# Performance work log

Hardware: AMD Instinct MI355X
Metric: run time of the kernel (lower is better)

## Reference

```python
import jax, jax.numpy as jnp
import numpy as np

SEQ = 512; WIN = [4, 4, 4]; INNER = 5; DM = 256; H = 4; DK = 64; NEG = -1e9

def _all_sizes():
    s = [SEQ]
    for w in WIN:
        s.append(s[-1] // w)
    return s

def _build_mask():
    # Pyraformer get_mask: intra-scale band (inner_size) + inter-scale parent/child links.
    sizes = _all_sizes(); N = sum(sizes)
    starts = np.cumsum([0] + sizes)
    allow = np.zeros((N, N), bool)
    iw = INNER // 2
    for li, sz in enumerate(sizes):
        st = int(starts[li])
        for i in range(st, st + sz):
            allow[i, max(i - iw, st):min(i + iw + 1, st + sz)] = True
    for li in range(1, len(sizes)):
        st = int(starts[li])
        for i in range(st, st + sizes[li]):
            ls = int(starts[li - 1]) + (i - st) * WIN[li - 1]
            rs = st if i == st + sizes[li] - 1 else int(starts[li - 1]) + (i - st + 1) * WIN[li - 1]
            allow[i, ls:rs] = True
            allow[ls:rs, i] = True
    return jnp.asarray(~allow)  # True = blocked

def _build_indexes():
    # Pyraformer refer_points: for each base position, index of its node at every scale.
    sizes = _all_sizes(); starts = np.cumsum([0] + sizes)
    idx = np.zeros((SEQ, len(sizes)), np.int32)
    for i in range(SEQ):
        cur = i
        idx[i, 0] = cur
        for j in range(1, len(sizes)):
            inner = cur - int(starts[j - 1])
            cur = int(starts[j]) + min(inner // WIN[j - 1], sizes[j] - 1)
            idx[i, j] = cur
    return jnp.asarray(idx)

def _pos_enc(L, D):
    pos = np.arange(L)[:, None]
    div = np.exp(np.arange(0, D, 2) * (-np.log(10000.0) / D))
    pe = np.zeros((L, D), np.float32)
    pe[:, 0::2] = np.sin(pos * div)
    pe[:, 1::2] = np.cos(pos * div)
    return jnp.asarray(pe)

MASK = _build_mask()
INDEXES = _build_indexes()
PE = _pos_enc(SEQ, DM)
DN = ('NCH', 'OIH', 'NCH')

def _ln(x, g, b, eps=1e-5):
    m = x.mean(-1, keepdims=True)
    v = ((x - m) ** 2).mean(-1, keepdims=True)
    return (x - m) * jax.lax.rsqrt(v + eps) * g + b

def _forward(x_enc, x_mark, W_val, W_time, b_time, W_down, b_down, W_conv, b_conv, bn_g, bn_b, W_up, b_up, ln_c_g, ln_c_b, Wq, bq, Wk, bk, Wv, bv, Wo, bo, ln1_g, ln1_b, W1f, b1f, W2f, b2f, ln2_g, ln2_b, Wp, bp):
    B = x_enc.shape[0]
    # DataEmbedding: circular k=3 token conv + time-feature linear + fixed positional
    xt = jnp.pad(x_enc.transpose(0, 2, 1), ((0, 0), (0, 0), (1, 1)), mode='wrap')
    val = jax.lax.conv_general_dilated(xt, W_val, (1,), 'VALID', dimension_numbers=DN).transpose(0, 2, 1)
    emb = val + x_mark @ W_time + b_time + PE[None]  # [B, SEQ, DM]
    # CSCM Bottleneck_Construct: down-proj, strided conv pooling per scale, up-proj, concat, LN
    t = (emb @ W_down + b_down).transpose(0, 2, 1)  # [B, 64, SEQ]
    pooled = []
    for i in range(len(WIN)):
        t = jax.lax.conv_general_dilated(t, W_conv[i], (WIN[i],), 'VALID', dimension_numbers=DN) + b_conv[i][None, :, None]
        t = jax.nn.elu(t * bn_g[i][None, :, None] + bn_b[i][None, :, None])
        pooled.append(t)
    pooled = jnp.concatenate(pooled, axis=2).transpose(0, 2, 1) @ W_up + b_up  # [B, 168, DM]
    x = _ln(jnp.concatenate([emb, pooled], axis=1), ln_c_g, ln_c_b)  # [B, 680, DM]
    N = x.shape[1]
    scale = np.float32(1.0 / np.sqrt(DK))
    for l in range(Wq.shape[0]):
        q = (x @ Wq[l] + bq[l]).reshape(B, N, H, DK).transpose(0, 2, 1, 3)
        k = (x @ Wk[l] + bk[l]).reshape(B, N, H, DK).transpose(0, 2, 1, 3)
        v = (x @ Wv[l] + bv[l]).reshape(B, N, H, DK).transpose(0, 2, 1, 3)
        s = jnp.einsum('bhqd,bhkd->bhqk', q, k) * scale
        s = jnp.where(MASK[None, None], NEG, s)
        o = jnp.einsum('bhqk,bhkd->bhqd', jax.nn.softmax(s, axis=-1), v)
        o = o.transpose(0, 2, 1, 3).reshape(B, N, DM) @ Wo[l] + bo[l]
        x = _ln(x + o, ln1_g[l], ln1_b[l])  # post-norm (normalize_before=False)
        f = jax.nn.relu(x @ W1f[l] + b1f[l]) @ W2f[l] + b2f[l]
        x = _ln(x + f, ln2_g[l], ln2_b[l])
    # FC decoder path: gather each position's multi-scale nodes, concat features
    gathered = x[:, INDEXES.reshape(-1)].reshape(B, SEQ, -1)  # [B, SEQ, 4*DM]
    return gathered[:, -1] @ Wp + bp  # [B, 96]

def setup_inputs() -> dict:
    key = jax.random.key(0)
    ks = iter(jax.random.split(key, 64))
    def w(shape, s=0.05):
        return jax.random.normal(next(ks), shape, jnp.float32) * s
    d = {}
    d['x_enc'] = jax.random.normal(next(ks), (32, SEQ, 1), jnp.float32)
    d['x_mark'] = jax.random.normal(next(ks), (32, SEQ, 4), jnp.float32)
    d['W_val'] = w((DM, 1, 3))
    d['W_time'] = w((4, DM)); d['b_time'] = jnp.zeros((DM,), jnp.float32)
    d['W_down'] = w((DM, 64)); d['b_down'] = jnp.zeros((64,), jnp.float32)
    d['W_conv'] = w((3, 64, 64, 4)); d['b_conv'] = jnp.zeros((3, 64), jnp.float32)
    d['bn_g'] = jnp.ones((3, 64), jnp.float32); d['bn_b'] = jnp.zeros((3, 64), jnp.float32)
    d['W_up'] = w((64, DM)); d['b_up'] = jnp.zeros((DM,), jnp.float32)
    d['ln_c_g'] = jnp.ones((DM,), jnp.float32); d['ln_c_b'] = jnp.zeros((DM,), jnp.float32)
    d['Wq'] = w((2, DM, DM)); d['bq'] = jnp.zeros((2, DM), jnp.float32)
    d['Wk'] = w((2, DM, DM)); d['bk'] = jnp.zeros((2, DM), jnp.float32)
    d['Wv'] = w((2, DM, DM)); d['bv'] = jnp.zeros((2, DM), jnp.float32)
    d['Wo'] = w((2, DM, DM)); d['bo'] = jnp.zeros((2, DM), jnp.float32)
    d['ln1_g'] = jnp.ones((2, DM), jnp.float32); d['ln1_b'] = jnp.zeros((2, DM), jnp.float32)
    d['W1f'] = w((2, DM, 512)); d['b1f'] = jnp.zeros((2, 512), jnp.float32)
    d['W2f'] = w((2, 512, DM)); d['b2f'] = jnp.zeros((2, DM), jnp.float32)
    d['ln2_g'] = jnp.ones((2, DM), jnp.float32); d['ln2_b'] = jnp.zeros((2, DM), jnp.float32)
    d['Wp'] = w((4 * DM, 96)); d['bp'] = jnp.zeros((96,), jnp.float32)
    return d

def reference(x_enc, x_mark, W_val, W_time, b_time, W_down, b_down, W_conv, b_conv, bn_g, bn_b, W_up, b_up, ln_c_g, ln_c_b, Wq, bq, Wk, bk, Wv, bv, Wo, bo, ln1_g, ln1_b, W1f, b1f, W2f, b2f, ln2_g, ln2_b, Wp, bp):
    return _forward(x_enc, x_mark, W_val, W_time, b_time, W_down, b_down, W_conv, b_conv, bn_g, bn_b, W_up, b_up, ln_c_g, ln_c_b, Wq, bq, Wk, bk, Wv, bv, Wo, bo, ln1_g, ln1_b, W1f, b1f, W2f, b2f, ln2_g, ln2_b, Wp, bp)
```

## Files before the change

kernel.cpp:

```cpp
#include <hip/hip_runtime.h>
#include <hip/hip_bf16.h>
#include <math.h>

#define B 32
#define SEQ 512
#define NTOK 680
#define DM 256
#define FF 512
#define NROWS (B*NTOK)

using bf16x8 = __attribute__((ext_vector_type(8))) short;
using f32x4  = __attribute__((ext_vector_type(4))) float;
using u32x4  = __attribute__((ext_vector_type(4))) unsigned int;
typedef __hip_bfloat16 bf16;

__device__ __forceinline__ unsigned short f2bf(float f) {
    union { float f; unsigned u; } x; x.f = f;
    unsigned r = (x.u + 0x7fffu + ((x.u >> 16) & 1u)) >> 16;
    return (unsigned short)r;
}
__device__ __forceinline__ float bfu2f(unsigned short u) {
    union { unsigned u; float f; } x; x.u = ((unsigned)u) << 16;
    return x.f;
}
__device__ __forceinline__ void dotu(unsigned a, unsigned b, float& s) {
    union { unsigned u; float f; } al, ah, bl, bh;
    al.u = a << 16; ah.u = a & 0xffff0000u;
    bl.u = b << 16; bh.u = b & 0xffff0000u;
    s = fmaf(al.f, bl.f, s);
    s = fmaf(ah.f, bh.f, s);
}

__global__ __launch_bounds__(256) void emb_kernel(
    const float* __restrict__ x_enc, const float* __restrict__ x_mark,
    const float* __restrict__ W_val, const float* __restrict__ W_time,
    const float* __restrict__ b_time, float* __restrict__ X, bf16* __restrict__ Xe)
{
    int bs = blockIdx.x;
    int b = bs >> 9, s = bs & 511;
    int d = threadIdx.x;
    int sm1 = (s + 511) & 511, sp1 = (s + 1) & 511;
    float x0 = x_enc[b*512 + sm1];
    float x1 = x_enc[b*512 + s];
    float x2 = x_enc[b*512 + sp1];
    float val = x0 * W_val[d*3+0] + x1 * W_val[d*3+1] + x2 * W_val[d*3+2];
    const float* mk = &x_mark[(size_t)bs*4];
    float tm = mk[0]*W_time[d] + mk[1]*W_time[256+d] + mk[2]*W_time[512+d] + mk[3]*W_time[768+d];
    int i2 = d & ~1;
    float div = expf((float)i2 * (-9.210340371976184f / 256.0f));
    float ang = (float)s * div;
    float pe = (d & 1) ? cosf(ang) : sinf(ang);
    float out = val + tm + b_time[d] + pe;
    X[((size_t)(b*NTOK + s))*DM + d] = out;
    ((unsigned short*)Xe)[(size_t)bs*DM + d] = f2bf(out);
}

__global__ __launch_bounds__(64) void conv_kernel(
    const float* __restrict__ in, int inRPB, int inOff,
    float* __restrict__ Pool, int outOff, int Lout,
    const float* __restrict__ W_conv, const float* __restrict__ b_conv,
    const float* __restrict__ bn_g, const float* __restrict__ bn_b, int sc)
{
    __shared__ float lds[256];
    int blk = blockIdx.x;
    int b = blk / Lout, p = blk % Lout;
    int t = threadIdx.x;
    for (int u = t; u < 256; u += 64)
        lds[u] = in[((size_t)(b*inRPB + inOff + p*4 + (u >> 6)))*64 + (u & 63)];
    __syncthreads();
    float acc = b_conv[sc*64 + t];
    const float* w = &W_conv[(size_t)(sc*64 + t)*256];
    #pragma unroll 4
    for (int ci = 0; ci < 64; ++ci) {
        #pragma unroll
        for (int tap = 0; tap < 4; ++tap)
            acc = fmaf(lds[tap*64 + ci], w[ci*4 + tap], acc);
    }
    float v = acc * bn_g[sc*64 + t] + bn_b[sc*64 + t];
    v = v > 0.f ? v : expm1f(v);
    Pool[((size_t)(b*168 + outOff + p))*64 + t] = v;
}

__global__ __launch_bounds__(256) void up_kernel(
    const float* __restrict__ Pool, const float* __restrict__ W_up,
    const float* __restrict__ b_up, float* __restrict__ X)
{
    __shared__ float row[64];
    int blk = blockIdx.x;
    int b = blk / 168, p = blk % 168;
    int d = threadIdx.x;
    if (d < 64) row[d] = Pool[(size_t)blk*64 + d];
    __syncthreads();
    float acc = b_up[d];
    #pragma unroll 8
    for (int k = 0; k < 64; ++k) acc = fmaf(row[k], W_up[k*256 + d], acc);
    X[((size_t)(b*NTOK + 512 + p))*DM + d] = acc;
}

__global__ __launch_bounds__(256) void ln_kernel(
    const float* __restrict__ Xf, bf16* __restrict__ Xio,
    const float* __restrict__ g, const float* __restrict__ bta)
{
    int r = blockIdx.x*4 + (threadIdx.x >> 6);
    int lane = threadIdx.x & 63;
    float4 v = ((const float4*)(Xf + (size_t)r*DM))[lane];
    float s = v.x + v.y + v.z + v.w;
    #pragma unroll
    for (int o = 32; o; o >>= 1) s += __shfl_xor(s, o);
    float mean = s * (1.0f/256.0f);
    float dx = v.x-mean, dy = v.y-mean, dz = v.z-mean, dw = v.w-mean;
    float q = dx*dx + dy*dy + dz*dz + dw*dw;
    #pragma unroll
    for (int o = 32; o; o >>= 1) q += __shfl_xor(q, o);
    float inv = rsqrtf(q*(1.0f/256.0f) + 1e-5f);
    float4 gg = ((const float4*)g)[lane];
    float4 bb = ((const float4*)bta)[lane];
    float ox = dx*inv*gg.x + bb.x;
    float oy = dy*inv*gg.y + bb.y;
    float oz = dz*inv*gg.z + bb.z;
    float ow = dw*inv*gg.w + bb.w;
    unsigned u0 = (unsigned)f2bf(ox) | ((unsigned)f2bf(oy) << 16);
    unsigned u1 = (unsigned)f2bf(oz) | ((unsigned)f2bf(ow) << 16);
    ((uint2*)(Xio + (size_t)r*DM))[lane] = make_uint2(u0, u1);
}

__global__ void nbr_kernel(int* __restrict__ nbr, int* __restrict__ ncnt)
{
    int i = blockIdx.x * 64 + threadIdx.x;
    if (i >= NTOK) return;
    const int starts[5] = {0, 512, 640, 672, 680};
    int si = (i < 512) ? 0 : (i < 640) ? 1 : (i < 672) ? 2 : 3;
    int st = starts[si], en = starts[si+1];
    int idx = i - st;
    int cnt = 0;
    if (si >= 1) {
        int cs = starts[si-1] + idx*4;
        #pragma unroll
        for (int c = 0; c < 4; ++c) nbr[i*16 + cnt++] = cs + c;
    }
    int lo = (i-2 > st) ? i-2 : st;
    int hi = (i+2 < en-1) ? i+2 : en-1;
    for (int j = lo; j <= hi; ++j) nbr[i*16 + cnt++] = j;
    if (si <= 2) nbr[i*16 + cnt++] = starts[si+1] + (idx >> 2);
    ncnt[i] = cnt;
}

__global__ __launch_bounds__(256) void attn_kernel(
    const bf16* __restrict__ Q, const bf16* __restrict__ K,
    const bf16* __restrict__ V, bf16* __restrict__ O,
    const int* __restrict__ nbr, const int* __restrict__ ncnt)
{
    __shared__ float wsm[4][16];
    __shared__ int   jsm[4][16];
    int flat = blockIdx.x;
    int row = (flat & 7) * (NROWS/8) + (flat >> 3);
    int n = row % NTOK, b = row / NTOK;
    int h = threadIdx.x >> 6;
    int lane = threadIdx.x & 63;
    int j = lane >> 2, g = lane & 3;
    int cnt = ncnt[n];
    int nj = (j < cnt) ? nbr[n*16 + j] : n;
    int jr = b*NTOK + nj;

    const uint4* qp = (const uint4*)(Q + (size_t)row*DM + h*64 + g*16);
    const uint4* kp = (const uint4*)(K + (size_t)jr*DM + h*64 + g*16);
    uint4 qa = qp[0], qb = qp[1];
    uint4 ka = kp[0], kb = kp[1];
    float s = 0.f;
    dotu(qa.x, ka.x, s); dotu(qa.y, ka.y, s); dotu(qa.z, ka.z, s); dotu(qa.w, ka.w, s);
    dotu(qb.x, kb.x, s); dotu(qb.y, kb.y, s); dotu(qb.z, kb.z, s); dotu(qb.w, kb.w, s);
    s += __shfl_xor(s, 1);
    s += __shfl_xor(s, 2);
    s *= 0.125f;
    if (j >= cnt) s = -1e30f;
    float m = s;
    #pragma unroll
    for (int o = 4; o < 64; o <<= 1) m = fmaxf(m, __shfl_xor(m, o));
    float w = (j < cnt) ? expf(s - m) : 0.f;
    float den = w;
    #pragma unroll
    for (int o = 4; o < 64; o <<= 1) den += __shfl_xor(den, o);
    if (g == 0) { wsm[h][j] = w / den; jsm[h][j] = jr; }
    __syncthreads();

    float acc = 0.f;
    const unsigned short* Vu = (const unsigned short*)V;
    for (int jj = 0; jj < cnt; ++jj) {
        float wv = wsm[h][jj];
        int rr = jsm[h][jj];
        acc = fmaf(wv, bfu2f(Vu[(size_t)rr*DM + h*64 + lane]), acc);
    }
    ((unsigned short*)O)[(size_t)row*DM + h*64 + lane] = f2bf(acc);
}

struct WDesc { const float* src; bf16* dst; int K; int N; };
struct WTable { WDesc d[13]; };
__global__ __launch_bounds__(256) void wconv_kernel(WTable tbl)
{
    __shared__ float lds[32][33];
    WDesc ds = tbl.d[blockIdx.y];
    int ntn = ds.N >> 5;
    int ntiles = (ds.K >> 5) * ntn;
    int tile = blockIdx.x;
    if (tile >= ntiles) return;
    int k0 = (tile / ntn) * 32, n0 = (tile % ntn) * 32;
    int t = threadIdx.x;
    int r = t >> 3, c4 = (t & 7) * 4;
    float4 v = *(const float4*)(ds.src + (size_t)(k0 + r)*ds.N + n0 + c4);
    lds[r][c4+0] = v.x; lds[r][c4+1] = v.y; lds[r][c4+2] = v.z; lds[r][c4+3] = v.w;
    __syncthreads();
    unsigned u0 = (unsigned)f2bf(lds[c4+0][r]) | ((unsigned)f2bf(lds[c4+1][r]) << 16);
    unsigned u1 = (unsigned)f2bf(lds[c4+2][r]) | ((unsigned)f2bf(lds[c4+3][r]) << 16);
    *(uint2*)((unsigned short*)ds.dst + (size_t)(n0 + r)*ds.K + k0 + c4) = make_uint2(u0, u1);
}

#define CSTR 260
__global__ __launch_bounds__(256) void wo_ln_kernel(
    const bf16* __restrict__ Ob, bf16* __restrict__ Xh,
    const bf16* __restrict__ WoT, const float* __restrict__ bo,
    const float* __restrict__ g, const float* __restrict__ bta)
{
    __shared__ __align__(16) char smem[16384 + 33280];
    uint4* AsU = (uint4*)smem;
    const bf16x8* Asv = (const bf16x8*)smem;
    float* ctile = (float*)(smem + 16384);

    int t = threadIdx.x;
    int lane = t & 63, w = t >> 6;
    int nwg = gridDim.x;
    int wg = (blockIdx.x & 7) * (nwg >> 3) + (blockIdx.x >> 3);
    int row0 = wg * 32;
    const unsigned short* Obu = (const unsigned short*)Ob;
    const unsigned short* Xu  = (const unsigned short*)Xh;
    const unsigned short* Wu  = (const unsigned short*)WoT;

    #pragma unroll
    for (int i = 0; i < 4; ++i) {
        int gg = t + i*256, r = gg >> 5, c = gg & 31;
        AsU[r*32 + (c ^ (r & 7))] = *(const uint4*)(Obu + (size_t)(row0 + r)*DM + c*8);
    }

    f32x4 acc[2][4];
    #pragma unroll
    for (int m = 0; m < 2; ++m)
        #pragma unroll
        for (int nn = 0; nn < 4; ++nn)
            #pragma unroll
            for (int q = 0; q < 4; ++q) acc[m][nn][q] = 0.f;
    float bv[4];
    #pragma unroll
    for (int nn = 0; nn < 4; ++nn) bv[nn] = bo[w*64 + nn*16 + (lane & 15)];
    __syncthreads();

    #pragma unroll
    for (int kt = 0; kt < 256; kt += 32) {
        int cg = (kt >> 3) + (lane >> 4);
        bf16x8 af[2];
        #pragma unroll
        for (int m = 0; m < 2; ++m) {
            int ar = m*16 + (lane & 15);
            af[m] = Asv[ar*32 + (cg ^ (ar & 7))];
        }
        #pragma unroll
        for (int nn = 0; nn < 4; ++nn) {
            int nrow = w*64 + nn*16 + (lane & 15);
            bf16x8 bfr = *(const bf16x8*)(Wu + (size_t)nrow*256 + kt + (lane >> 4)*8);
            #pragma unroll
            for (int m = 0; m < 2; ++m)
                acc[m][nn] = __builtin_amdgcn_mfma_f32_16x16x32_bf16(af[m], bfr, acc[m][nn], 0, 0, 0);
        }
    }

    __syncthreads();
    #pragma unroll
    for (int m = 0; m < 2; ++m)
        #pragma unroll
        for (int nn = 0; nn < 4; ++nn) {
            int col = w*64 + nn*16 + (lane & 15);
            #pragma unroll
            for (int q = 0; q < 4; ++q) {
                int row = m*16 + (lane >> 4)*4 + q;
                ctile[row*CSTR + col] = acc[m][nn][q] + bv[nn];
            }
        }
    __syncthreads();
    #pragma unroll
    for (int rr = 0; rr < 8; ++rr) {
        int row = w*8 + rr;
        float4 v = *(const float4*)(ctile + row*CSTR + lane*4);
        uint2 xu = *(const uint2*)(Xu + (size_t)(row0 + row)*DM + lane*4);
        v.x += bfu2f((unsigned short)(xu.x & 0xffffu));
        v.y += bfu2f((unsigned short)(xu.x >> 16));
        v.z += bfu2f((unsigned short)(xu.y & 0xffffu));
        v.w += bfu2f((unsigned short)(xu.y >> 16));
        float s = v.x + v.y + v.z + v.w;
        #pragma unroll
        for (int o = 32; o; o >>= 1) s += __shfl_xor(s, o);
        float mean = s * (1.0f/256.0f);
        float dx = v.x-mean, dy = v.y-mean, dz = v.z-mean, dw = v.w-mean;
        float q2 = dx*dx + dy*dy + dz*dz + dw*dw;
        #pragma unroll
        for (int o = 32; o; o >>= 1) q2 += __shfl_xor(q2, o);
        float inv = rsqrtf(q2*(1.0f/256.0f) + 1e-5f);
        float4 gg = ((const float4*)g)[lane];
        float4 bb = ((const float4*)bta)[lane];
        float ox = dx*inv*gg.x + bb.x;
        float oy = dy*inv*gg.y + bb.y;
        float oz = dz*inv*gg.z + bb.z;
        float ow = dw*inv*gg.w + bb.w;
        unsigned u0 = (unsigned)f2bf(ox) | ((unsigned)f2bf(oy) << 16);
        unsigned u1 = (unsigned)f2bf(oz) | ((unsigned)f2bf(ow) << 16);
        *(uint2*)((unsigned short*)Xh + (size_t)(row0 + row)*DM + lane*4) = make_uint2(u0, u1);
    }
}

#define HSTR 280
__global__ __launch_bounds__(256) void ff_kernel(
    bf16* __restrict__ Xh,
    const bf16* __restrict__ W1t, const float* __restrict__ b1,
    const bf16* __restrict__ W2t, const float* __restrict__ b2,
    const float* __restrict__ g, const float* __restrict__ bta)
{
    __shared__ __align__(16) char smem[16384 + 33280];
    uint4* AsU = (uint4*)smem;
    const bf16x8* Asv = (const bf16x8*)smem;
    unsigned short* hT = (unsigned short*)(smem + 16384);
    float* ctile = (float*)(smem + 16384);

    int t = threadIdx.x;
    int lane = t & 63, w = t >> 6;
    int nwg = gridDim.x;
    int wg = (blockIdx.x & 7) * (nwg >> 3) + (blockIdx.x >> 3);
    int row0 = wg * 32;
    const unsigned short* Xu = (const unsigned short*)Xh;

    #pragma unroll
    for (int i = 0; i < 4; ++i) {
        int gg = t + i*256, r = gg >> 5, c = gg & 31;
        AsU[r*32 + (c ^ (r & 7))] = *(const uint4*)(Xu + (size_t)(row0 + r)*DM + c*8);
    }

    f32x4 acc2[2][4];
    #pragma unroll
    for (int m = 0; m < 2; ++m)
        #pragma unroll
        for (int nn = 0; nn < 4; ++nn)
            #pragma unroll
            for (int q = 0; q < 4; ++q) acc2[m][nn][q] = 0.f;
    float b2v[4];
    #pragma unroll
    for (int nn = 0; nn < 4; ++nn) b2v[nn] = b2[w*64 + nn*16 + (lane & 15)];
    __syncthreads();

    const unsigned short* W1u = (const unsigned short*)W1t;
    const unsigned short* W2u = (const unsigned short*)W2t;

    #pragma unroll
    for (int half = 0; half < 2; ++half) {
        f32x4 acc1[2][4];
        #pragma unroll
        for (int m = 0; m < 2; ++m)
            #pragma unroll
            for (int nn = 0; nn < 4; ++nn)
                #pragma unroll
                for (int q = 0; q < 4; ++q) acc1[m][nn][q] = 0.f;
        #pragma unroll
        for (int kt = 0; kt < 256; kt += 32) {
            int cg = (kt >> 3) + (lane >> 4);
            bf16x8 af[2];
            #pragma unroll
            for (int m = 0; m < 2; ++m) {
                int ar = m*16 + (lane & 15);
                af[m] = Asv[ar*32 + (cg ^ (ar & 7))];
            }
            #pragma unroll
            for (int nn = 0; nn < 4; ++nn) {
                int nrow = half*256 + w*64 + nn*16 + (lane & 15);
                bf16x8 bfr = *(const bf16x8*)(W1u + (size_t)nrow*256 + kt + (lane >> 4)*8);
                #pragma unroll
                for (int m = 0; m < 2; ++m)
                    acc1[m][nn] = __builtin_amdgcn_mfma_f32_16x16x32_bf16(af[m], bfr, acc1[m][nn], 0, 0, 0);
            }
        }
        float b1v[4];
        #pragma unroll
        for (int nn = 0; nn < 4; ++nn) b1v[nn] = b1[half*256 + w*64 + nn*16 + (lane & 15)];
        __syncthreads();
        #pragma unroll
        for (int m = 0; m < 2; ++m)
            #pragma unroll
            for (int nn = 0; nn < 4; ++nn) {
                int col = w*64 + nn*16 + (lane & 15);
                #pragma unroll
                for (int q = 0; q < 4; ++q) {
                    int row = m*16 + (lane >> 4)*4 + q;
                    hT[row*HSTR + col] = f2bf(fmaxf(acc1[m][nn][q] + b1v[nn], 0.f));
                }
            }
        __syncthreads();
        #pragma unroll
        for (int kt = 0; kt < 256; kt += 32) {
            bf16x8 af[2];
            #pragma unroll
            for (int m = 0; m < 2; ++m) {
                int ar = m*16 + (lane & 15);
                af[m] = *(const bf16x8*)(hT + ar*HSTR + kt + (lane >> 4)*8);
            }
            #pragma unroll
            for (int nn = 0; nn < 4; ++nn) {
                int nrow = w*64 + nn*16 + (lane & 15);
                bf16x8 bfr = *(const bf16x8*)(W2u + (size_t)nrow*512 + half*256 + kt + (lane >> 4)*8);
                #pragma unroll
                for (int m = 0; m < 2; ++m)
                    acc2[m][nn] = __builtin_amdgcn_mfma_f32_16x16x32_bf16(af[m], bfr, acc2[m][nn], 0, 0, 0);
            }
        }
    }
    __syncthreads();
    #pragma unroll
    for (int m = 0; m < 2; ++m)
        #pragma unroll
        for (int nn = 0; nn < 4; ++nn) {
            int col = w*64 + nn*16 + (lane & 15);
            #pragma unroll
            for (int q = 0; q < 4; ++q) {
                int row = m*16 + (lane >> 4)*4 + q;
                ctile[row*CSTR + col] = acc2[m][nn][q] + b2v[nn];
            }
        }
    __syncthreads();
    #pragma unroll
    for (int rr = 0; rr < 8; ++rr) {
        int row = w*8 + rr;
        float4 v = *(const float4*)(ctile + row*CSTR + lane*4);
        uint2 xu = *(const uint2*)(Xu + (size_t)(row0 + row)*DM + lane*4);
        v.x += bfu2f((unsigned short)(xu.x & 0xffffu));
        v.y += bfu2f((unsigned short)(xu.x >> 16));
        v.z += bfu2f((unsigned short)(xu.y & 0xffffu));
        v.w += bfu2f((unsigned short)(xu.y >> 16));
        float s = v.x + v.y + v.z + v.w;
        #pragma unroll
        for (int o = 32; o; o >>= 1) s += __shfl_xor(s, o);
        float mean = s * (1.0f/256.0f);
        float dx = v.x-mean, dy = v.y-mean, dz = v.z-mean, dw = v.w-mean;
        float q2 = dx*dx + dy*dy + dz*dz + dw*dw;
        #pragma unroll
        for (int o = 32; o; o >>= 1) q2 += __shfl_xor(q2, o);
        float inv = rsqrtf(q2*(1.0f/256.0f) + 1e-5f);
        float4 gg = ((const float4*)g)[lane];
        float4 bb = ((const float4*)bta)[lane];
        float ox = dx*inv*gg.x + bb.x;
        float oy = dy*inv*gg.y + bb.y;
        float oz = dz*inv*gg.z + bb.z;
        float ow = dw*inv*gg.w + bb.w;
        unsigned u0 = (unsigned)f2bf(ox) | ((unsigned)f2bf(oy) << 16);
        unsigned u1 = (unsigned)f2bf(oz) | ((unsigned)f2bf(ow) << 16);
        *(uint2*)((unsigned short*)Xh + (size_t)(row0 + row)*DM + lane*4) = make_uint2(u0, u1);
    }
}

template<int KD, int NY, int NZ, bool RELU>
__global__ __launch_bounds__(256) void mfma_gemm_fr(
    const bf16* __restrict__ A,
    const bf16* __restrict__ Wt0, const bf16* __restrict__ Wt1, const bf16* __restrict__ Wt2,
    const float* __restrict__ b0, const float* __restrict__ b1, const float* __restrict__ b2,
    bf16* __restrict__ O0, bf16* __restrict__ O1, bf16* __restrict__ O2,
    int Nc, int totalWg)
{
    __shared__ __align__(16) char smem[40960];
    uint4* AsU = (uint4*)smem;
    uint4* BsU = (uint4*)(smem + 8192);
    const bf16x8* Asv = (const bf16x8*)smem;
    const bf16x8* Bsv = (const bf16x8*)(smem + 8192);

    int t = threadIdx.x;
    int lane = t & 63, wid = t >> 6;
    int nwg = gridDim.x;
    int wg = (blockIdx.x & 7) * (nwg >> 3) + (blockIdx.x >> 3);
    if (wg >= totalWg) return;
    int xt = wg / (NY*NZ);
    int rem = wg % (NY*NZ);
    int z = rem / NY;
    int y = rem % NY;
    int row0 = xt * 64;
    int n0 = y * 256;
    const bf16* W = ((z == 0) ? Wt0 : (z == 1) ? Wt1 : Wt2) + (size_t)n0*KD;
    const float* bias = (z == 0) ? b0 : (z == 1) ? b1 : b2;
    bf16* Op = (z == 0) ? O0 : (z == 1) ? O1 : O2;

    f32x4 acc[4][4];
    #pragma unroll
    for (int i = 0; i < 4; ++i)
        #pragma unroll
        for (int jn = 0; jn < 4; ++jn)
            #pragma unroll
            for (int r = 0; r < 4; ++r) acc[i][jn][r] = 0.f;

    uint4 pa[2], pb[8];
    #pragma unroll
    for (int i = 0; i < 2; ++i) {
        int gg = t + i*256, r = gg >> 3, c = gg & 7;
        pa[i] = *reinterpret_cast<const uint4*>(A + (size_t)(row0 + r)*KD + c*8);
    }
    #pragma unroll
    for (int i = 0; i < 8; ++i) {
        int gg = t + i*256, r = gg >> 3, c = gg & 7;
        pb[i] = *reinterpret_cast<const uint4*>(W + (size_t)r*KD + c*8);
    }

    #pragma unroll
    for (int kt = 0; kt < KD; kt += 64) {
        __syncthreads();
        #pragma unroll
        for (int i = 0; i < 2; ++i) {
            int gg = t + i*256, r = gg >> 3, c = gg & 7;
            AsU[r*8 + (c ^ (r & 7))] = pa[i];
        }
        #pragma unroll
        for (int i = 0; i < 8; ++i) {
            int gg = t + i*256, r = gg >> 3, c = gg & 7;
            BsU[r*8 + (c ^ (r & 7))] = pb[i];
        }
        __syncthreads();
        if (kt + 64 < KD) {
            #pragma unroll
            for (int i = 0; i < 2; ++i) {
                int gg = t + i*256, r = gg >> 3, c = gg & 7;
                pa[i] = *reinterpret_cast<const uint4*>(A + (size_t)(row0 + r)*KD + (kt + 64) + c*8);
            }
            #pragma unroll
            for (int i = 0; i < 8; ++i) {
                int gg = t + i*256, r = gg >> 3, c = gg & 7;
                pb[i] = *reinterpret_cast<const uint4*>(W + (size_t)r*KD + (kt + 64) + c*8);
            }
        }
        #pragma unroll
        for (int ks = 0; ks < 2; ++ks) {
            int cg = ks*4 + (lane >> 4);
            bf16x8 af[4], bfr[4];
            #pragma unroll
            for (int m = 0; m < 4; ++m) {
                int ar = m*16 + (lane & 15);
                af[m] = Asv[ar*8 + (cg ^ (ar & 7))];
            }
            #pragma unroll
            for (int nn = 0; nn < 4; ++nn) {
                int br = wid*64 + nn*16 + (lane & 15);
                bfr[nn] = Bsv[br*8 + (cg ^ (br & 7))];
            }
            #pragma unroll
            for (int m = 0; m < 4; ++m)
                #pragma unroll
                for (int nn = 0; nn < 4; ++nn)
                    acc[m][nn] = __builtin_amdgcn_mfma_f32_16x16x32_bf16(af[m], bfr[nn], acc[m][nn], 0, 0, 0);
        }
    }

    __syncthreads();
    unsigned short* ctb = (unsigned short*)smem;
    #pragma unroll
    for (int m = 0; m < 4; ++m) {
        #pragma unroll
        for (int nn = 0; nn < 4; ++nn) {
            int cc = wid*64 + nn*16 + (lane & 15);
            float bcol = bias[n0 + cc];
            #pragma unroll
            for (int r = 0; r < 4; ++r) {
                int rr = m*16 + (lane >> 4)*4 + r;
                float v = acc[m][nn][r] + bcol;
                if (RELU) v = fmaxf(v, 0.f);
                ctb[rr*264 + cc] = f2bf(v);
            }
        }
    }
    __syncthreads();
    #pragma unroll
    for (int i = 0; i < 8; ++i) {
        int idx = t + i*256;
        int row = idx >> 5, c16 = idx & 31;
        u32x4 uv = *(const u32x4*)(ctb + row*264 + c16*8);
        *(u32x4*)((unsigned short*)Op + (size_t)(row0 + row)*Nc + n0 + c16*8) = uv;
    }
}

__global__ __launch_bounds__(256) void mfma_gemm_dn(
    const bf16* __restrict__ A, const bf16* __restrict__ Wt,
    const float* __restrict__ bias, float* __restrict__ Op)
{
    __shared__ __align__(16) char smem[34816];
    uint4* AsU = (uint4*)smem;
    uint4* BsU = (uint4*)(smem + 16384);
    const bf16x8* Asv = (const bf16x8*)smem;
    const bf16x8* Bsv = (const bf16x8*)(smem + 16384);
    const int KD = 256, Nc = 64;

    int t = threadIdx.x;
    int lane = t & 63, wid = t >> 6;
    int wm = wid >> 1, wn = wid & 1;
    int nwg = gridDim.x;
    int wg = (blockIdx.x & 7) * (nwg >> 3) + (blockIdx.x >> 3);
    int row0 = wg * 128;
    int n0 = 0;

    f32x4 acc[4][2];
    #pragma unroll
    for (int i = 0; i < 4; ++i)
        #pragma unroll
        for (int jn = 0; jn < 2; ++jn)
            #pragma unroll
            for (int r = 0; r < 4; ++r) acc[i][jn][r] = 0.f;

    uint4 pa[4], pb[2];
    #pragma unroll
    for (int i = 0; i < 4; ++i) {
        int gg = t + i*256, r = gg >> 3, c = gg & 7;
        pa[i] = *reinterpret_cast<const uint4*>(A + (size_t)(row0 + r)*KD + c*8);
    }
    #pragma unroll
    for (int i = 0; i < 2; ++i) {
        int gg = t + i*256, r = gg >> 3, c = gg & 7;
        pb[i] = *reinterpret_cast<const uint4*>(Wt + (size_t)(n0 + r)*KD + c*8);
    }

    #pragma unroll
    for (int kt = 0; kt < KD; kt += 64) {
        __syncthreads();
        #pragma unroll
        for (int i = 0; i < 4; ++i) {
            int gg = t + i*256, r = gg >> 3, c = gg & 7;
            AsU[r*8 + (c ^ (r & 7))] = pa[i];
        }
        #pragma unroll
        for (int i = 0; i < 2; ++i) {
            int gg = t + i*256, r = gg >> 3, c = gg & 7;
            BsU[r*8 + (c ^ (r & 7))] = pb[i];
        }
        __syncthreads();
        if (kt + 64 < KD) {
            #pragma unroll
            for (int i = 0; i < 4; ++i) {
                int gg = t + i*256, r = gg >> 3, c = gg & 7;
                pa[i] = *reinterpret_cast<const uint4*>(A + (size_t)(row0 + r)*KD + (kt + 64) + c*8);
            }
            #pragma unroll
            for (int i = 0; i < 2; ++i) {
                int gg = t + i*256, r = gg >> 3, c = gg & 7;
                pb[i] = *reinterpret_cast<const uint4*>(Wt + (size_t)(n0 + r)*KD + (kt + 64) + c*8);
            }
        }
        #pragma unroll
        for (int ks = 0; ks < 2; ++ks) {
            int cg = ks*4 + (lane >> 4);
            bf16x8 af[4], bfr[2];
            #pragma unroll
            for (int m = 0; m < 4; ++m) {
                int ar = wm*64 + m*16 + (lane & 15);
                af[m] = Asv[ar*8 + (cg ^ (ar & 7))];
            }
            #pragma unroll
            for (int nn = 0; nn < 2; ++nn) {
                int br = wn*32 + nn*16 + (lane & 15);
                bfr[nn] = Bsv[br*8 + (cg ^ (br & 7))];
            }
            #pragma unroll
            for (int m = 0; m < 4; ++m)
                #pragma unroll
                for (int nn = 0; nn < 2; ++nn)
                    acc[m][nn] = __builtin_amdgcn_mfma_f32_16x16x32_bf16(af[m], bfr[nn], acc[m][nn], 0, 0, 0);
        }
    }

    __syncthreads();
    float* ctile = (float*)smem;
    #pragma unroll
    for (int m = 0; m < 4; ++m) {
        #pragma unroll
        for (int nn = 0; nn < 2; ++nn) {
            int cc = wn*32 + nn*16 + (lane & 15);
            float bcol = bias[n0 + cc];
            #pragma unroll
            for (int r = 0; r < 4; ++r) {
                int rr = wm*64 + m*16 + (lane >> 4)*4 + r;
                ctile[rr*68 + cc] = acc[m][nn][r] + bcol;
            }
        }
    }
    __syncthreads();
    int c4 = (t & 15) * 4;
    #pragma unroll
    for (int rr = t >> 4; rr < 128; rr += 16) {
        float4 v = *reinterpret_cast<const float4*>(ctile + rr*68 + c4);
        *reinterpret_cast<float4*>(Op + (size_t)(row0 + rr)*Nc + n0 + c4) = v;
    }
}

__global__ __launch_bounds__(128) void final_kernel(
    const bf16* __restrict__ Xh, const float* __restrict__ Wp,
    const float* __restrict__ bp, float* __restrict__ out)
{
    __shared__ float rows[1024];
    int b = blockIdx.x, t = threadIdx.x;
    const unsigned short* Xu = (const unsigned short*)Xh;
    for (int u = t; u < 1024; u += 128) {
        int g = u >> 8;
        int id = (g == 0) ? 511 : (g == 1) ? 639 : (g == 2) ? 671 : 679;
        rows[u] = bfu2f(Xu[((size_t)(b*NTOK + id))*DM + (u & 255)]);
    }
    __syncthreads();
    if (t < 96) {
        float acc = bp[t];
        #pragma unroll 8
        for (int k = 0; k < 1024; ++k) acc = fmaf(rows[k], Wp[k*96 + t], acc);
        out[b*96 + t] = acc;
    }
}

extern "C" void kernel_launch(void* const* d_in, const int* in_sizes, int n_in,
                              void* d_out, int out_size, void* d_ws, size_t ws_size,
                              hipStream_t stream)
{
    const float* x_enc  = (const float*)d_in[0];
    const float* x_mark = (const float*)d_in[1];
    const float* W_val  = (const float*)d_in[2];
    const float* W_time = (const float*)d_in[3];
    const float* b_time = (const float*)d_in[4];
    const float* W_down = (const float*)d_in[5];
    const float* b_down = (const float*)d_in[6];
    const float* W_conv = (const float*)d_in[7];
    const float* b_conv = (const float*)d_in[8];
    const float* bn_g   = (const float*)d_in[9];
    const float* bn_b   = (const float*)d_in[10];
    const float* W_up   = (const float*)d_in[11];
    const float* b_up   = (const float*)d_in[12];
    const float* ln_c_g = (const float*)d_in[13];
    const float* ln_c_b = (const float*)d_in[14];
    const float* Wq     = (const float*)d_in[15];
    const float* bq     = (const float*)d_in[16];
    const float* Wk     = (const float*)d_in[17];
    const float* bk     = (const float*)d_in[18];
    const float* Wv     = (const float*)d_in[19];
    const float* bv     = (const float*)d_in[20];
    const float* Wo     = (const float*)d_in[21];
    const float* bo     = (const float*)d_in[22];
    const float* ln1_g  = (const float*)d_in[23];
    const float* ln1_b  = (const float*)d_in[24];
    const float* W1f    = (const float*)d_in[25];
    const float* b1f    = (const float*)d_in[26];
    const float* W2f    = (const float*)d_in[27];
    const float* b2f    = (const float*)d_in[28];
    const float* ln2_g  = (const float*)d_in[29];
    const float* ln2_b  = (const float*)d_in[30];
    const float* Wp     = (const float*)d_in[31];
    const float* bp     = (const float*)d_in[32];

    const size_t RB = (size_t)NROWS * DM;
    float* ws = (float*)d_ws;
    float* X    = ws;
    float* Td   = X + RB;
    float* Pool = Td + (size_t)B*SEQ*64;
    bf16* bws   = (bf16*)(Pool + (size_t)B*168*64);
    bf16* Xh   = bws;
    bf16* Qh   = Xh  + RB;
    bf16* Kh   = Qh  + RB;
    bf16* Vh   = Kh  + RB;
    bf16* Obh  = Vh  + RB;
    bf16* Xe   = Obh + RB;
    bf16* WqT  = Xe  + (size_t)B*SEQ*DM;
    bf16* WkT  = WqT + 2*65536;
    bf16* WvT  = WkT + 2*65536;
    bf16* WoT  = WvT + 2*65536;
    bf16* W1T  = WoT + 2*65536;
    bf16* W2T  = W1T + 2*131072;
    bf16* WdT  = W2T + 2*131072;
    int*  nbr  = (int*)(WdT + 64*256);
    int*  ncnt = nbr + NTOK*16;

    WTable tbl;
    for (int l = 0; l < 2; ++l) {
        tbl.d[l*6+0] = { Wq  + (size_t)l*65536,  WqT + (size_t)l*65536,  256, 256 };
        tbl.d[l*6+1] = { Wk  + (size_t)l*65536,  WkT + (size_t)l*65536,  256, 256 };
        tbl.d[l*6+2] = { Wv  + (size_t)l*65536,  WvT + (size_t)l*65536,  256, 256 };
        tbl.d[l*6+3] = { Wo  + (size_t)l*65536,  WoT + (size_t)l*65536,  256, 256 };
        tbl.d[l*6+4] = { W1f + (size_t)l*131072, W1T + (size_t)l*131072, 256, 512 };
        tbl.d[l*6+5] = { W2f + (size_t)l*131072, W2T + (size_t)l*131072, 512, 256 };
    }
    tbl.d[12] = { W_down, WdT, 256, 64 };
    wconv_kernel<<<dim3(128, 13), 256, 0, stream>>>(tbl);

    emb_kernel<<<B*SEQ, 256, 0, stream>>>(x_enc, x_mark, W_val, W_time, b_time, X, Xe);
    mfma_gemm_dn<<<128, 256, 0, stream>>>(Xe, WdT, b_down, Td);
    conv_kernel<<<B*128, 64, 0, stream>>>(Td, 512, 0,   Pool, 0,   128, W_conv, b_conv, bn_g, bn_b, 0);
    conv_kernel<<<B*32,  64, 0, stream>>>(Pool, 168, 0,  Pool, 128, 32,  W_conv, b_conv, bn_g, bn_b, 1);
    conv_kernel<<<B*8,   64, 0, stream>>>(Pool, 168, 128,Pool, 160, 8,   W_conv, b_conv, bn_g, bn_b, 2);
    up_kernel<<<B*168, 256, 0, stream>>>(Pool, W_up, b_up, X);
    ln_kernel<<<NROWS/4, 256, 0, stream>>>(X, Xh, ln_c_g, ln_c_b);
    nbr_kernel<<<11, 64, 0, stream>>>(nbr, ncnt);

    const int MT = NROWS/64;
    for (int l = 0; l < 2; ++l) {
        const bf16* wqt = WqT + (size_t)l*65536;
        const bf16* wkt = WkT + (size_t)l*65536;
        const bf16* wvt = WvT + (size_t)l*65536;
        const bf16* wot = WoT + (size_t)l*65536;
        const bf16* w1t = W1T + (size_t)l*131072;
        const bf16* w2t = W2T + (size_t)l*131072;
        const float* bq_ = bq + l*DM; const float* bk_ = bk + l*DM;
        const float* bv_ = bv + l*DM; const float* bo_ = bo + l*DM;
        const float* b1_ = b1f + l*FF; const float* b2_ = b2f + l*DM;

        mfma_gemm_fr<256,1,3,false><<<1024, 256, 0, stream>>>(
            Xh, wqt, wkt, wvt, bq_, bk_, bv_, Qh, Kh, Vh, 256, MT*3);
        attn_kernel<<<NROWS, 256, 0, stream>>>(Qh, Kh, Vh, Obh, nbr, ncnt);
        wo_ln_kernel<<<680, 256, 0, stream>>>(Obh, Xh, wot, bo_, ln1_g + l*DM, ln1_b + l*DM);
        ff_kernel<<<680, 256, 0, stream>>>(Xh, w1t, b1_, w2t, b2_, ln2_g + l*DM, ln2_b + l*DM);
    }

    final_kernel<<<B, 128, 0, stream>>>(Xh, Wp, bp, (float*)d_out);
}
```

Measured before the change: 471.0 us.

## Fold Wv·Wo per head and fuse attention with output projection and LN

```diff
diff --git a/kernel.cpp b/kernel.cpp
--- a/kernel.cpp
+++ b/kernel.cpp
@@ -145,56 +145,8 @@
     ncnt[i] = cnt;
 }
 
-__global__ __launch_bounds__(256) void attn_kernel(
-    const bf16* __restrict__ Q, const bf16* __restrict__ K,
-    const bf16* __restrict__ V, bf16* __restrict__ O,
-    const int* __restrict__ nbr, const int* __restrict__ ncnt)
-{
-    __shared__ float wsm[4][16];
-    __shared__ int   jsm[4][16];
-    int flat = blockIdx.x;
-    int row = (flat & 7) * (NROWS/8) + (flat >> 3);
-    int n = row % NTOK, b = row / NTOK;
-    int h = threadIdx.x >> 6;
-    int lane = threadIdx.x & 63;
-    int j = lane >> 2, g = lane & 3;
-    int cnt = ncnt[n];
-    int nj = (j < cnt) ? nbr[n*16 + j] : n;
-    int jr = b*NTOK + nj;
-
-    const uint4* qp = (const uint4*)(Q + (size_t)row*DM + h*64 + g*16);
-    const uint4* kp = (const uint4*)(K + (size_t)jr*DM + h*64 + g*16);
-    uint4 qa = qp[0], qb = qp[1];
-    uint4 ka = kp[0], kb = kp[1];
-    float s = 0.f;
-    dotu(qa.x, ka.x, s); dotu(qa.y, ka.y, s); dotu(qa.z, ka.z, s); dotu(qa.w, ka.w, s);
-    dotu(qb.x, kb.x, s); dotu(qb.y, kb.y, s); dotu(qb.z, kb.z, s); dotu(qb.w, kb.w, s);
-    s += __shfl_xor(s, 1);
-    s += __shfl_xor(s, 2);
-    s *= 0.125f;
-    if (j >= cnt) s = -1e30f;
-    float m = s;
-    #pragma unroll
-    for (int o = 4; o < 64; o <<= 1) m = fmaxf(m, __shfl_xor(m, o));
-    float w = (j < cnt) ? expf(s - m) : 0.f;
-    float den = w;
-    #pragma unroll
-    for (int o = 4; o < 64; o <<= 1) den += __shfl_xor(den, o);
-    if (g == 0) { wsm[h][j] = w / den; jsm[h][j] = jr; }
-    __syncthreads();
-
-    float acc = 0.f;
-    const unsigned short* Vu = (const unsigned short*)V;
-    for (int jj = 0; jj < cnt; ++jj) {
-        float wv = wsm[h][jj];
-        int rr = jsm[h][jj];
-        acc = fmaf(wv, bfu2f(Vu[(size_t)rr*DM + h*64 + lane]), acc);
-    }
-    ((unsigned short*)O)[(size_t)row*DM + h*64 + lane] = f2bf(acc);
-}
-
 struct WDesc { const float* src; bf16* dst; int K; int N; };
-struct WTable { WDesc d[13]; };
+struct WTable { WDesc d[9]; };
 __global__ __launch_bounds__(256) void wconv_kernel(WTable tbl)
 {
     __shared__ float lds[32][33];
@@ -214,31 +166,103 @@
     *(uint2*)((unsigned short*)ds.dst + (size_t)(n0 + r)*ds.K + k0 + c4) = make_uint2(u0, u1);
 }
 
+__global__ __launch_bounds__(256) void wvo_kernel(
+    const float* __restrict__ Wv, const float* __restrict__ Wo, bf16* __restrict__ WvoT)
+{
+    int lh = blockIdx.y; int l = lh >> 2, h = lh & 3;
+    int e = blockIdx.x*256 + threadIdx.x;
+    int n = e >> 8, k = e & 255;
+    const float* wv = Wv + (size_t)l*65536 + k*256 + h*64;
+    const float* wo = Wo + (size_t)l*65536 + (h*64)*256 + n;
+    float acc = 0.f;
+    #pragma unroll 8
+    for (int m = 0; m < 64; ++m) acc = fmaf(wv[m], wo[m*256], acc);
+    ((unsigned short*)WvoT)[(size_t)lh*65536 + n*256 + k] = f2bf(acc);
+}
+
+__global__ void fvec_kernel(const float* __restrict__ bv, const float* __restrict__ Wo,
+                            const float* __restrict__ bo, float* __restrict__ fvec)
+{
+    int l = blockIdx.x, n = threadIdx.x;
+    const float* bvl = bv + l*256;
+    const float* wol = Wo + (size_t)l*65536;
+    float acc = bo[l*256 + n];
+    for (int c = 0; c < 256; ++c) acc = fmaf(bvl[c], wol[c*256 + n], acc);
+    fvec[l*256 + n] = acc;
+}
+
+#define HSTR 280
 #define CSTR 260
-__global__ __launch_bounds__(256) void wo_ln_kernel(
-    const bf16* __restrict__ Ob, bf16* __restrict__ Xh,
-    const bf16* __restrict__ WoT, const float* __restrict__ bo,
-    const float* __restrict__ g, const float* __restrict__ bta)
-{
-    __shared__ __align__(16) char smem[16384 + 33280];
-    uint4* AsU = (uint4*)smem;
-    const bf16x8* Asv = (const bf16x8*)smem;
-    float* ctile = (float*)(smem + 16384);
+__global__ __launch_bounds__(256) void attn_full_kernel(
+    const bf16* __restrict__ Qh, const bf16* __restrict__ Kh,
+    const bf16* __restrict__ Xin, bf16* __restrict__ Xout,
+    const bf16* __restrict__ WvoT,
+    const float* __restrict__ fvec,
+    const float* __restrict__ g, const float* __restrict__ bta,
+    const int* __restrict__ nbr, const int* __restrict__ ncnt)
+{
+    __shared__ __align__(16) char smem[33280 + 8192 + 2048 + 128];
+    unsigned short* Ysm = (unsigned short*)smem;
+    float* ctile = (float*)smem;
+    float* Psm  = (float*)(smem + 33280);
+    int* jrowS  = (int*)(smem + 33280 + 8192);
+    int* cntS   = (int*)(smem + 33280 + 8192 + 2048);
 
     int t = threadIdx.x;
-    int lane = t & 63, w = t >> 6;
+    int w = t >> 6, lane = t & 63;
     int nwg = gridDim.x;
     int wg = (blockIdx.x & 7) * (nwg >> 3) + (blockIdx.x >> 3);
     int row0 = wg * 32;
-    const unsigned short* Obu = (const unsigned short*)Ob;
-    const unsigned short* Xu  = (const unsigned short*)Xh;
-    const unsigned short* Wu  = (const unsigned short*)WoT;
-
-    #pragma unroll
-    for (int i = 0; i < 4; ++i) {
-        int gg = t + i*256, r = gg >> 5, c = gg & 31;
-        AsU[r*32 + (c ^ (r & 7))] = *(const uint4*)(Obu + (size_t)(row0 + r)*DM + c*8);
-    }
+    const unsigned short* Qu = (const unsigned short*)Qh;
+    const unsigned short* Ku = (const unsigned short*)Kh;
+    const unsigned short* Xu = (const unsigned short*)Xin;
+    const unsigned short* Wu = (const unsigned short*)WvoT;
+
+    if (t < 32) cntS[t] = ncnt[(row0 + t) % NTOK];
+    #pragma unroll
+    for (int i = 0; i < 2; ++i) {
+        int idx = t + i*256, r = idx >> 4, s = idx & 15;
+        int grow = row0 + r;
+        int n = grow % NTOK, b = grow / NTOK;
+        int c = ncnt[n];
+        jrowS[r*16 + s] = (s < c) ? (b*NTOK + nbr[n*16 + s]) : grow;
+    }
+    __syncthreads();
+
+    {
+        int s = lane >> 2, gd = lane & 3;
+        for (int rr = 0; rr < 8; ++rr) {
+            int r = w*8 + rr, grow = row0 + r;
+            int cnt = cntS[r];
+            int jr = jrowS[r*16 + s];
+            bool valid = s < cnt;
+            #pragma unroll
+            for (int h = 0; h < 4; ++h) {
+                const uint4* qp = (const uint4*)(Qu + (size_t)grow*DM + h*64 + gd*16);
+                const uint4* kp = (const uint4*)(Ku + (size_t)jr*DM + h*64 + gd*16);
+                uint4 qa = qp[0], qb = qp[1];
+                uint4 ka = kp[0], kb = kp[1];
+                float sv = 0.f;
+                dotu(qa.x, ka.x, sv); dotu(qa.y, ka.y, sv);
+                dotu(qa.z, ka.z, sv); dotu(qa.w, ka.w, sv);
+                dotu(qb.x, kb.x, sv); dotu(qb.y, kb.y, sv);
+                dotu(qb.z, kb.z, sv); dotu(qb.w, kb.w, sv);
+                sv += __shfl_xor(sv, 1);
+                sv += __shfl_xor(sv, 2);
+                sv *= 0.125f;
+                if (!valid) sv = -1e30f;
+                float m = sv;
+                #pragma unroll
+                for (int o = 4; o < 64; o <<= 1) m = fmaxf(m, __shfl_xor(m, o));
+                float p = valid ? expf(sv - m) : 0.f;
+                float den = p;
+                #pragma unroll
+                for (int o = 4; o < 64; o <<= 1) den += __shfl_xor(den, o);
+                if (gd == 0) Psm[(r*4 + h)*16 + s] = p / den;
+            }
+        }
+    }
+    __syncthreads();
 
     f32x4 acc[2][4];
     #pragma unroll
@@ -247,31 +271,63 @@
         for (int nn = 0; nn < 4; ++nn)
             #pragma unroll
             for (int q = 0; q < 4; ++q) acc[m][nn][q] = 0.f;
-    float bv[4];
-    #pragma unroll
-    for (int nn = 0; nn < 4; ++nn) bv[nn] = bo[w*64 + nn*16 + (lane & 15)];
-    __syncthreads();
-
-    #pragma unroll
-    for (int kt = 0; kt < 256; kt += 32) {
-        int cg = (kt >> 3) + (lane >> 4);
-        bf16x8 af[2];
-        #pragma unroll
-        for (int m = 0; m < 2; ++m) {
-            int ar = m*16 + (lane & 15);
-            af[m] = Asv[ar*32 + (cg ^ (ar & 7))];
-        }
-        #pragma unroll
-        for (int nn = 0; nn < 4; ++nn) {
-            int nrow = w*64 + nn*16 + (lane & 15);
-            bf16x8 bfr = *(const bf16x8*)(Wu + (size_t)nrow*256 + kt + (lane >> 4)*8);
-            #pragma unroll
-            for (int m = 0; m < 2; ++m)
-                acc[m][nn] = __builtin_amdgcn_mfma_f32_16x16x32_bf16(af[m], bfr, acc[m][nn], 0, 0, 0);
-        }
-    }
-
-    __syncthreads();
+
+    int rY = t >> 3, dg = t & 7;
+    #pragma unroll
+    for (int h = 0; h < 4; ++h) {
+        float y[32];
+        #pragma unroll
+        for (int q = 0; q < 32; ++q) y[q] = 0.f;
+        int cnt = cntS[rY];
+        for (int sI = 0; sI < cnt; ++sI) {
+            float p = Psm[(rY*4 + h)*16 + sI];
+            int jr = jrowS[rY*16 + sI];
+            const uint4* xp = (const uint4*)(Xu + (size_t)jr*DM + dg*32);
+            #pragma unroll
+            for (int c = 0; c < 4; ++c) {
+                uint4 xv = xp[c];
+                unsigned uu[4] = {xv.x, xv.y, xv.z, xv.w};
+                #pragma unroll
+                for (int q = 0; q < 4; ++q) {
+                    y[c*8 + 2*q+0] = fmaf(p, bfu2f((unsigned short)(uu[q] & 0xffffu)), y[c*8 + 2*q+0]);
+                    y[c*8 + 2*q+1] = fmaf(p, bfu2f((unsigned short)(uu[q] >> 16)),     y[c*8 + 2*q+1]);
+                }
+            }
+        }
+        #pragma unroll
+        for (int c = 0; c < 4; ++c) {
+            u32x4 pk;
+            pk[0] = (unsigned)f2bf(y[c*8+0]) | ((unsigned)f2bf(y[c*8+1]) << 16);
+            pk[1] = (unsigned)f2bf(y[c*8+2]) | ((unsigned)f2bf(y[c*8+3]) << 16);
+            pk[2] = (unsigned)f2bf(y[c*8+4]) | ((unsigned)f2bf(y[c*8+5]) << 16);
+            pk[3] = (unsigned)f2bf(y[c*8+6]) | ((unsigned)f2bf(y[c*8+7]) << 16);
+            *(u32x4*)(Ysm + rY*HSTR + dg*32 + c*8) = pk;
+        }
+        __syncthreads();
+        const unsigned short* Wh = Wu + (size_t)h*65536;
+        #pragma unroll
+        for (int kt = 0; kt < 256; kt += 32) {
+            bf16x8 af[2];
+            #pragma unroll
+            for (int m = 0; m < 2; ++m) {
+                int ar = m*16 + (lane & 15);
+                af[m] = *(const bf16x8*)(Ysm + ar*HSTR + kt + (lane >> 4)*8);
+            }
+            #pragma unroll
+            for (int nn = 0; nn < 4; ++nn) {
+                int nrow = w*64 + nn*16 + (lane & 15);
+                bf16x8 bfr = *(const bf16x8*)(Wh + (size_t)nrow*256 + kt + (lane >> 4)*8);
+                #pragma unroll
+                for (int m = 0; m < 2; ++m)
+                    acc[m][nn] = __builtin_amdgcn_mfma_f32_16x16x32_bf16(af[m], bfr, acc[m][nn], 0, 0, 0);
+            }
+        }
+        __syncthreads();
+    }
+
+    float fv[4];
+    #pragma unroll
+    for (int nn = 0; nn < 4; ++nn) fv[nn] = fvec[w*64 + nn*16 + (lane & 15)];
     #pragma unroll
     for (int m = 0; m < 2; ++m)
         #pragma unroll
@@ -280,7 +336,7 @@
             #pragma unroll
             for (int q = 0; q < 4; ++q) {
                 int row = m*16 + (lane >> 4)*4 + q;
-                ctile[row*CSTR + col] = acc[m][nn][q] + bv[nn];
+                ctile[row*CSTR + col] = acc[m][nn][q] + fv[nn];
             }
         }
     __syncthreads();
@@ -310,11 +366,10 @@
         float ow = dw*inv*gg.w + bb.w;
         unsigned u0 = (unsigned)f2bf(ox) | ((unsigned)f2bf(oy) << 16);
         unsigned u1 = (unsigned)f2bf(oz) | ((unsigned)f2bf(ow) << 16);
-        *(uint2*)((unsigned short*)Xh + (size_t)(row0 + row)*DM + lane*4) = make_uint2(u0, u1);
-    }
-}
-
-#define HSTR 280
+        *(uint2*)((unsigned short*)Xout + (size_t)(row0 + row)*DM + lane*4) = make_uint2(u0, u1);
+    }
+}
+
 __global__ __launch_bounds__(256) void ff_kernel(
     bf16* __restrict__ Xh,
     const bf16* __restrict__ W1t, const float* __restrict__ b1,
@@ -758,34 +813,33 @@
     float* X    = ws;
     float* Td   = X + RB;
     float* Pool = Td + (size_t)B*SEQ*64;
-    bf16* bws   = (bf16*)(Pool + (size_t)B*168*64);
+    float* fvec = Pool + (size_t)B*168*64;
+    bf16* bws   = (bf16*)(fvec + 512);
     bf16* Xh   = bws;
-    bf16* Qh   = Xh  + RB;
+    bf16* Xh2  = Xh  + RB;
+    bf16* Qh   = Xh2 + RB;
     bf16* Kh   = Qh  + RB;
-    bf16* Vh   = Kh  + RB;
-    bf16* Obh  = Vh  + RB;
-    bf16* Xe   = Obh + RB;
+    bf16* Xe   = Kh  + RB;
     bf16* WqT  = Xe  + (size_t)B*SEQ*DM;
     bf16* WkT  = WqT + 2*65536;
-    bf16* WvT  = WkT + 2*65536;
-    bf16* WoT  = WvT + 2*65536;
-    bf16* W1T  = WoT + 2*65536;
+    bf16* W1T  = WkT + 2*65536;
     bf16* W2T  = W1T + 2*131072;
     bf16* WdT  = W2T + 2*131072;
-    int*  nbr  = (int*)(WdT + 64*256);
+    bf16* WvoT = WdT + 64*256;
+    int*  nbr  = (int*)(WvoT + 8*65536);
     int*  ncnt = nbr + NTOK*16;
 
     WTable tbl;
     for (int l = 0; l < 2; ++l) {
-        tbl.d[l*6+0] = { Wq  + (size_t)l*65536,  WqT + (size_t)l*65536,  256, 256 };
-        tbl.d[l*6+1] = { Wk  + (size_t)l*65536,  WkT + (size_t)l*65536,  256, 256 };
-        tbl.d[l*6+2] = { Wv  + (size_t)l*65536,  WvT + (size_t)l*65536,  256, 256 };
-        tbl.d[l*6+3] = { Wo  + (size_t)l*65536,  WoT + (size_t)l*65536,  256, 256 };
-        tbl.d[l*6+4] = { W1f + (size_t)l*131072, W1T + (size_t)l*131072, 256, 512 };
-        tbl.d[l*6+5] = { W2f + (size_t)l*131072, W2T + (size_t)l*131072, 512, 256 };
-    }
-    tbl.d[12] = { W_down, WdT, 256, 64 };
-    wconv_kernel<<<dim3(128, 13), 256, 0, stream>>>(tbl);
+        tbl.d[l*4+0] = { Wq  + (size_t)l*65536,  WqT + (size_t)l*65536,  256, 256 };
+        tbl.d[l*4+1] = { Wk  + (size_t)l*65536,  WkT + (size_t)l*65536,  256, 256 };
+        tbl.d[l*4+2] = { W1f + (size_t)l*131072, W1T + (size_t)l*131072, 256, 512 };
+        tbl.d[l*4+3] = { W2f + (size_t)l*131072, W2T + (size_t)l*131072, 512, 256 };
+    }
+    tbl.d[8] = { W_down, WdT, 256, 64 };
+    wconv_kernel<<<dim3(128, 9), 256, 0, stream>>>(tbl);
+    wvo_kernel<<<dim3(256, 8), 256, 0, stream>>>(Wv, Wo, WvoT);
+    fvec_kernel<<<2, 256, 0, stream>>>(bv, Wo, bo, fvec);
 
     emb_kernel<<<B*SEQ, 256, 0, stream>>>(x_enc, x_mark, W_val, W_time, b_time, X, Xe);
     mfma_gemm_dn<<<128, 256, 0, stream>>>(Xe, WdT, b_down, Td);
@@ -797,23 +851,24 @@
     nbr_kernel<<<11, 64, 0, stream>>>(nbr, ncnt);
 
     const int MT = NROWS/64;
+    bf16* Xa = Xh;
+    bf16* Xb = Xh2;
     for (int l = 0; l < 2; ++l) {
         const bf16* wqt = WqT + (size_t)l*65536;
         const bf16* wkt = WkT + (size_t)l*65536;
-        const bf16* wvt = WvT + (size_t)l*65536;
-        const bf16* wot = WoT + (size_t)l*65536;
         const bf16* w1t = W1T + (size_t)l*131072;
         const bf16* w2t = W2T + (size_t)l*131072;
         const float* bq_ = bq + l*DM; const float* bk_ = bk + l*DM;
-        const float* bv_ = bv + l*DM; const float* bo_ = bo + l*DM;
         const float* b1_ = b1f + l*FF; const float* b2_ = b2f + l*DM;
 
-        mfma_gemm_fr<256,1,3,false><<<1024, 256, 0, stream>>>(
-            Xh, wqt, wkt, wvt, bq_, bk_, bv_, Qh, Kh, Vh, 256, MT*3);
-        attn_kernel<<<NROWS, 256, 0, stream>>>(Qh, Kh, Vh, Obh, nbr, ncnt);
-        wo_ln_kernel<<<680, 256, 0, stream>>>(Obh, Xh, wot, bo_, ln1_g + l*DM, ln1_b + l*DM);
-        ff_kernel<<<680, 256, 0, stream>>>(Xh, w1t, b1_, w2t, b2_, ln2_g + l*DM, ln2_b + l*DM);
-    }
-
-    final_kernel<<<B, 128, 0, stream>>>(Xh, Wp, bp, (float*)d_out);
-}
+        mfma_gemm_fr<256,1,2,false><<<680, 256, 0, stream>>>(
+            Xa, wqt, wkt, wqt, bq_, bk_, bq_, Qh, Kh, Qh, 256, MT*2);
+        attn_full_kernel<<<680, 256, 0, stream>>>(
+            Qh, Kh, Xa, Xb, WvoT + (size_t)l*4*65536, fvec + l*256,
+            ln1_g + l*DM, ln1_b + l*DM, nbr, ncnt);
+        ff_kernel<<<680, 256, 0, stream>>>(Xb, w1t, b1_, w2t, b2_, ln2_g + l*DM, ln2_b + l*DM);
+        bf16* tmp = Xa; Xa = Xb; Xb = tmp;
+    }
+
+    final_kernel<<<B, 128, 0, stream>>>(Xa, Wp, bp, (float*)d_out);
+}
```

After: 578.5 us. +22.8%, slower.
